# Optimization experiments

Measured on AMD Instinct MI355X. Metric: run time of the kernel, lower is better.

Reference implementation:

```python
import jax, jax.numpy as jnp
import numpy as np

NUM_HIST = 4
INTERVAL = 5
PROG_THRESH = 2.0

B = 32          # scenarios
AGENTS_PER = 10 # agents per scenario
A = B * AGENTS_PER
T = 32          # future intervals
P = 20000       # polylines
NG = 2000       # polygons
L = 180         # raw trajectory length (L//INTERVAL = 36 >= T+1)


def setup_inputs() -> dict:
    key = jax.random.key(0)
    ks = jax.random.split(key, 8)
    polyline_batch = jnp.sort(jax.random.randint(ks[0], (P,), 0, B, dtype=jnp.int32))
    polyline_position = jax.random.normal(ks[1], (P, 2), dtype=jnp.float32) * 50.0
    polyline_heading = jax.random.uniform(ks[2], (P,), dtype=jnp.float32) * 2.0 * np.pi
    edge_row1 = jax.random.randint(ks[3], (P,), 0, NG, dtype=jnp.int32)
    polyline_to_polygon_edge_index = jnp.stack([jnp.arange(P, dtype=jnp.int32), edge_row1])
    polygon_on_route_mask = jax.random.randint(ks[4], (NG,), 0, 2) > 0
    agent_ptr = (jnp.arange(B + 1, dtype=jnp.int32) * AGENTS_PER)
    agent_infer_position = jax.random.normal(ks[5], (A, NUM_HIST + T, 2), dtype=jnp.float32) * 50.0
    agent_batch = jnp.repeat(jnp.arange(B, dtype=jnp.int32), AGENTS_PER)
    agent_position = jax.random.normal(ks[6], (A, L, 2), dtype=jnp.float32) * 50.0
    return {
        "polyline_batch": polyline_batch,
        "polyline_position": polyline_position,
        "polyline_heading": polyline_heading,
        "polyline_to_polygon_edge_index": polyline_to_polygon_edge_index,
        "polygon_on_route_mask": polygon_on_route_mask,
        "agent_ptr": agent_ptr,
        "agent_infer_position": agent_infer_position,
        "agent_batch": agent_batch,
        "agent_position": agent_position,
    }


def _local_x(points, centers, cos_h, sin_h):
    # points [E,2]; centers [P,2]; returns x_local, y_local each [E,P]
    dx = points[:, None, 0] - centers[None, :, 0]
    dy = points[:, None, 1] - centers[None, :, 1]
    x = cos_h[None, :] * dx + sin_h[None, :] * dy
    y = -sin_h[None, :] * dx + cos_h[None, :] * dy
    return x, y


def _progress(pos, pos_pre, pos_batch, poly_pos, cos_h, sin_h, on_route, poly_batch, t):
    # dense equivalent of mask-build -> dense_to_sparse -> gather -> scatter_min
    x, y = _local_x(pos, poly_pos, cos_h, sin_h)          # [E,P]
    x_pre, _ = _local_x(pos_pre, poly_pos, cos_h, sin_h)  # [E,P]
    dist = jnp.abs(y) * 10.0 + jnp.abs(x) + jnp.where(x > 0, 1000.0, 0.0)
    valid = on_route[None, :] & (pos_batch[:, None] == poly_batch[None, :])
    dist = jnp.where(valid, dist, jnp.inf)
    j = jnp.argmin(dist, axis=1)                          # first-min, matches scatter_min
    has = jnp.any(valid, axis=1)
    x_sel = jnp.take_along_axis(x, j[:, None], axis=1)[:, 0]
    x_pre_sel = jnp.take_along_axis(x_pre, j[:, None], axis=1)[:, 0]
    prog = jnp.where(has, x_sel - x_pre_sel, 0.0)
    return prog.reshape(-1, t).sum(axis=-1)


def reference(polyline_batch, polyline_position, polyline_heading,
              polyline_to_polygon_edge_index, polygon_on_route_mask,
              agent_ptr, agent_infer_position, agent_batch, agent_position):
    poly_on_route = polygon_on_route_mask[polyline_to_polygon_edge_index[1]]
    cos_h = jnp.cos(polyline_heading)
    sin_h = jnp.sin(polyline_heading)

    ego_index = agent_ptr[:-1]
    ip = agent_infer_position[ego_index]                  # [B, NUM_HIST+T, 2]
    t = ip.shape[1] - NUM_HIST
    ego_pos = ip[:, NUM_HIST:].reshape(-1, 2)
    ego_pos_pre = ip[:, NUM_HIST - 1:-1].reshape(-1, 2)
    ego_b = jnp.repeat(agent_batch[ego_index], t)

    progress = _progress(ego_pos, ego_pos_pre, ego_b, polyline_position,
                         cos_h, sin_h, poly_on_route, polyline_batch, t)

    expert = agent_position[ego_index, ::INTERVAL]        # [B, L//INTERVAL, 2]
    expert_pre = expert[:, -t - 1:-1].reshape(-1, 2)
    expert_cur = expert[:, -t:].reshape(-1, 2)
    expert_progress = _progress(expert_cur, expert_pre, ego_b, polyline_position,
                                cos_h, sin_h, poly_on_route, polyline_batch, t)

    reward = jnp.minimum(
        jnp.maximum(progress, PROG_THRESH) / jnp.maximum(expert_progress, PROG_THRESH),
        1.0)
    return reward
```

## Files before the change

### kernel.cpp

```cpp
#include <hip/hip_runtime.h>

#define NUM_HIST 4
#define T_STEPS 32
#define B_BATCH 32
#define L_LEN 180
#define INTERVAL 5
#define CHUNK 2048
#define BT 1024

__global__ __launch_bounds__(BT) void fused_progress_reward(
    const int* __restrict__ pb,
    const float* __restrict__ pp,
    const float* __restrict__ hd,
    const int* __restrict__ edge,
    const unsigned int* __restrict__ mask,
    const int* __restrict__ aptr,
    const float* __restrict__ ipos,
    const int* __restrict__ abatch,
    const float* __restrict__ apos,
    float* __restrict__ out,
    int P)
{
    __shared__ float4 stage[CHUNK];
    __shared__ float progv[64];
    __shared__ int starts_sh[B_BATCH + 1];
    __shared__ int wcnt[16], woff[16];
    __shared__ int ccount_sh;

    const int tid = threadIdx.x;
    const int b   = blockIdx.x;

    bool bytemode = false;
    #pragma unroll
    for (int w = 0; w < 16; ++w) bytemode |= (mask[w] & 0xFFFFFF00u) != 0u;

    const int a  = aptr[b];
    const int bq = abatch[a];

    {
        int base = tid * 20;
        if (base < P) {
            int prev = (base == 0) ? -1 : pb[base - 1];
            int lim  = min(base + 20, P);
            for (int k = base; k + 3 < lim; k += 4) {
                int4 v4 = *(const int4*)(pb + k);
                int vals[4] = {v4.x, v4.y, v4.z, v4.w};
                #pragma unroll
                for (int u = 0; u < 4; ++u) {
                    int v = min(vals[u], B_BATCH);
                    for (int t = prev + 1; t <= v; ++t) starts_sh[t] = k + u;
                    prev = v;
                }
            }
            if (lim == P) {
                for (int t = prev + 1; t <= B_BATCH; ++t) starts_sh[t] = P;
            }
        }
        if (tid == 0) ccount_sh = 0;
    }

    const int qid = tid >> 4;
    const int sub = tid & 15;
    const int s   = qid >> 5;
    const int ts  = qid & 31;

    float cx, cy, px_, py_;
    if (s == 0) {
        const float2* base2 = (const float2*)(ipos + (size_t)a * ((NUM_HIST + T_STEPS) * 2));
        float2 pre = base2[NUM_HIST - 1 + ts];
        float2 cur = base2[NUM_HIST + ts];
        cx = cur.x; cy = cur.y; px_ = pre.x; py_ = pre.y;
    } else {
        const float2* base2 = (const float2*)(apos + (size_t)a * (L_LEN * 2));
        float2 pre = base2[(3 + ts) * INTERVAL];
        float2 cur = base2[(4 + ts) * INTERVAL];
        cx = cur.x; cy = cur.y; px_ = pre.x; py_ = pre.y;
    }

    __syncthreads();
    const int jb = starts_sh[bq];
    const int je = starts_sh[bq + 1];

    unsigned long long best = ~0ull;
    float bc = 0.0f, bs = 0.0f;
    int keybase = 0;

    const unsigned long long lt_mask = (1ull << (tid & 63)) - 1ull;

    for (int c0 = jb; c0 < je; c0 += CHUNK) {
        const int n = min(CHUNK, je - c0);

        for (int r0 = 0; r0 < n; r0 += BT) {
            int i = r0 + tid;
            bool on = false;
            float4 v;
            if (i < n) {
                int j = c0 + i;
                int g = edge[P + j];
                on = bytemode ? (((const unsigned char*)mask)[g] != 0)
                              : (mask[g] != 0u);
                float h  = hd[j];
                float cc = __cosf(h);
                float sn = __sinf(h);
                float2 p2 = ((const float2*)pp)[j];
                v = make_float4(cc, sn, cc * p2.x + sn * p2.y,
                                        -sn * p2.x + cc * p2.y);
            }
            unsigned long long bal = __ballot(on);
            int within = __popcll(bal & lt_mask);
            if ((tid & 63) == 0) wcnt[tid >> 6] = (int)__popcll(bal);
            __syncthreads();
            if (tid < 16) {
                int c = wcnt[tid];
                int p = c;
                #pragma unroll
                for (int off = 1; off < 16; off <<= 1) {
                    int t = __shfl_up(p, off, 64);
                    if (tid >= off) p += t;
                }
                int basev = ccount_sh;
                woff[tid] = basev + p - c;
                if (tid == 15) ccount_sh = basev + p;
            }
            __syncthreads();
            if (on) stage[woff[tid >> 6] + within] = v;
        }
        __syncthreads();
        const int nc = ccount_sh;

        for (int i = sub; i < nc; i += 16) {
            float4 e = stage[i];
            float x = e.x * cx + e.y * cy - e.z;
            float y = -e.y * cx + e.x * cy - e.w;
            float d = fabsf(y) * 10.0f + fabsf(x) + (x > 0.0f ? 1000.0f : 0.0f);
            unsigned long long cand =
                ((unsigned long long)__float_as_uint(d) << 32)
                | (unsigned int)(keybase + i);
            if (cand < best) { best = cand; bc = e.x; bs = e.y; }
        }
        keybase += nc;
        if (c0 + CHUNK < je) {
            __syncthreads();
            if (tid == 0) ccount_sh = 0;
        }
    }

    #pragma unroll
    for (int off = 1; off < 16; off <<= 1) {
        unsigned long long b2 = __shfl_xor(best, off, 64);
        float c2 = __shfl_xor(bc, off, 64);
        float s2 = __shfl_xor(bs, off, 64);
        if (b2 < best) { best = b2; bc = c2; bs = s2; }
    }

    if (sub == 0) {
        float prog = 0.0f;
        if (best != ~0ull)
            prog = bc * (cx - px_) + bs * (cy - py_);
        progv[qid] = prog;
    }
    __syncthreads();

    if (tid < 64) {
        float v = progv[tid];
        #pragma unroll
        for (int off = 16; off; off >>= 1) v += __shfl_xor(v, off, 64);
        float other = __shfl_xor(v, 32, 64);
        if (tid == 0)
            out[b] = fminf(fmaxf(v, 2.0f) / fmaxf(other, 2.0f), 1.0f);
    }
}

extern "C" void kernel_launch(void* const* d_in, const int* in_sizes, int n_in,
                              void* d_out, int out_size, void* d_ws, size_t ws_size,
                              hipStream_t stream) {
    const int*   poly_batch  = (const int*)d_in[0];
    const float* poly_pos    = (const float*)d_in[1];
    const float* heading     = (const float*)d_in[2];
    const int*   edge        = (const int*)d_in[3];
    const unsigned int* mask = (const unsigned int*)d_in[4];
    const int*   agent_ptr   = (const int*)d_in[5];
    const float* ipos        = (const float*)d_in[6];
    const int*   agent_batch = (const int*)d_in[7];
    const float* apos        = (const float*)d_in[8];
    float* out = (float*)d_out;

    const int P = in_sizes[0];

    fused_progress_reward<<<B_BATCH, BT, 0, stream>>>(
        poly_batch, poly_pos, heading, edge, mask,
        agent_ptr, ipos, agent_batch, apos, out, P);
}
```

Measured before the change: 75.38 us.

## Split into grid-wide prep kernel and lightweight per-scenario eval kernel

Moves the polyline transform, mask lookup and segment-start computation into a separate kernel that runs over all polylines with many blocks, writing transformed float4 records to workspace. Off-route polylines get a sentinel value that pushes their distance far above any real candidate, so the in-block ballot/prefix-sum compaction and its repeated barriers go away. The eval kernel then scans each scenario's range straight from global memory using 512 threads, 8 lanes per query. It recovers the heading from the winning index instead of carrying cos/sin through the reduction. The cost is a second launch and a workspace round trip, and the sentinel changes tie-breaking indices to global ones.

```diff
diff --git a/kernel.cpp b/kernel.cpp
--- a/kernel.cpp
+++ b/kernel.cpp
@@ -5,159 +5,116 @@
 #define B_BATCH 32
 #define L_LEN 180
 #define INTERVAL 5
-#define CHUNK 2048
-#define BT 1024
+#define PREP_BT 256
+#define EVAL_BT 512
 
-__global__ __launch_bounds__(BT) void fused_progress_reward(
+typedef unsigned long long u64;
+typedef unsigned int u32;
+
+__global__ __launch_bounds__(PREP_BT) void prep_kernel(
     const int* __restrict__ pb,
     const float* __restrict__ pp,
     const float* __restrict__ hd,
     const int* __restrict__ edge,
     const unsigned int* __restrict__ mask,
-    const int* __restrict__ aptr,
-    const float* __restrict__ ipos,
-    const int* __restrict__ abatch,
-    const float* __restrict__ apos,
-    float* __restrict__ out,
+    int* __restrict__ starts,
+    float4* __restrict__ tf,
     int P)
 {
-    __shared__ float4 stage[CHUNK];
-    __shared__ float progv[64];
-    __shared__ int starts_sh[B_BATCH + 1];
-    __shared__ int wcnt[16], woff[16];
-    __shared__ int ccount_sh;
-
-    const int tid = threadIdx.x;
-    const int b   = blockIdx.x;
-
     bool bytemode = false;
     #pragma unroll
     for (int w = 0; w < 16; ++w) bytemode |= (mask[w] & 0xFFFFFF00u) != 0u;
 
-    const int a  = aptr[b];
+    const int j = blockIdx.x * PREP_BT + threadIdx.x;
+    if (j >= P) return;
+
+    int g = edge[P + j];
+    bool on = bytemode ? (((const unsigned char*)mask)[g] != 0)
+                       : (mask[g] != 0u);
+    float4 v;
+    if (on) {
+        float h  = hd[j];
+        float cc = __cosf(h);
+        float sn = __sinf(h);
+        float2 p2 = ((const float2*)pp)[j];
+        v = make_float4(cc, sn, cc * p2.x + sn * p2.y,
+                                -sn * p2.x + cc * p2.y);
+    } else {
+        v = make_float4(0.0f, 0.0f, -3e30f, 0.0f);
+    }
+    tf[j] = v;
+
+    int val = min(pb[j], B_BATCH);
+    int pv  = (j == 0) ? -1 : min(pb[j - 1], B_BATCH);
+    for (int t = pv + 1; t <= val; ++t) starts[t] = j;
+    if (j == P - 1)
+        for (int t = val + 1; t <= B_BATCH; ++t) starts[t] = P;
+}
+
+__global__ __launch_bounds__(EVAL_BT) void eval_final_kernel(
+    const float4* __restrict__ tf,
+    const int* __restrict__ starts,
+    const int* __restrict__ aptr,
+    const int* __restrict__ abatch,
+    const float* __restrict__ ipos,
+    const float* __restrict__ apos,
+    const float* __restrict__ hd,
+    float* __restrict__ out)
+{
+    __shared__ float progv[64];
+
+    const int tid = threadIdx.x;
+    const int b   = blockIdx.x;
+    const int q   = tid >> 3;
+    const int sub = tid & 7;
+    const int s   = q >> 5;
+    const int ts  = q & 31;
+
+    const int a = aptr[b];
+    float2 pre, cur;
+    if (s == 0) {
+        const float2* b2 =
+            (const float2*)(ipos + (size_t)a * ((NUM_HIST + T_STEPS) * 2));
+        pre = b2[NUM_HIST - 1 + ts];
+        cur = b2[NUM_HIST + ts];
+    } else {
+        const float2* b2 = (const float2*)(apos + (size_t)a * (L_LEN * 2));
+        pre = b2[(3 + ts) * INTERVAL];
+        cur = b2[(4 + ts) * INTERVAL];
+    }
+    const float cx = cur.x, cy = cur.y;
+
     const int bq = abatch[a];
+    const int jb = starts[bq];
+    const int je = starts[bq + 1];
 
-    {
-        int base = tid * 20;
-        if (base < P) {
-            int prev = (base == 0) ? -1 : pb[base - 1];
-            int lim  = min(base + 20, P);
-            for (int k = base; k + 3 < lim; k += 4) {
-                int4 v4 = *(const int4*)(pb + k);
-                int vals[4] = {v4.x, v4.y, v4.z, v4.w};
-                #pragma unroll
-                for (int u = 0; u < 4; ++u) {
-                    int v = min(vals[u], B_BATCH);
-                    for (int t = prev + 1; t <= v; ++t) starts_sh[t] = k + u;
-                    prev = v;
-                }
-            }
-            if (lim == P) {
-                for (int t = prev + 1; t <= B_BATCH; ++t) starts_sh[t] = P;
-            }
-        }
-        if (tid == 0) ccount_sh = 0;
+    u64 best = ~0ull;
+    #pragma unroll 8
+    for (int i = jb + sub; i < je; i += 8) {
+        float4 e = tf[i];
+        float x =  e.x * cx + e.y * cy - e.z;
+        float y = -e.y * cx + e.x * cy - e.w;
+        float d = fabsf(y) * 10.0f + fabsf(x) + (x > 0.0f ? 1000.0f : 0.0f);
+        u64 cand = ((u64)__float_as_uint(d) << 32) | (u32)i;
+        if (cand < best) best = cand;
     }
 
-    const int qid = tid >> 4;
-    const int sub = tid & 15;
-    const int s   = qid >> 5;
-    const int ts  = qid & 31;
-
-    float cx, cy, px_, py_;
-    if (s == 0) {
-        const float2* base2 = (const float2*)(ipos + (size_t)a * ((NUM_HIST + T_STEPS) * 2));
-        float2 pre = base2[NUM_HIST - 1 + ts];
-        float2 cur = base2[NUM_HIST + ts];
-        cx = cur.x; cy = cur.y; px_ = pre.x; py_ = pre.y;
-    } else {
-        const float2* base2 = (const float2*)(apos + (size_t)a * (L_LEN * 2));
-        float2 pre = base2[(3 + ts) * INTERVAL];
-        float2 cur = base2[(4 + ts) * INTERVAL];
-        cx = cur.x; cy = cur.y; px_ = pre.x; py_ = pre.y;
-    }
-
-    __syncthreads();
-    const int jb = starts_sh[bq];
-    const int je = starts_sh[bq + 1];
-
-    unsigned long long best = ~0ull;
-    float bc = 0.0f, bs = 0.0f;
-    int keybase = 0;
-
-    const unsigned long long lt_mask = (1ull << (tid & 63)) - 1ull;
-
-    for (int c0 = jb; c0 < je; c0 += CHUNK) {
-        const int n = min(CHUNK, je - c0);
-
-        for (int r0 = 0; r0 < n; r0 += BT) {
-            int i = r0 + tid;
-            bool on = false;
-            float4 v;
-            if (i < n) {
-                int j = c0 + i;
-                int g = edge[P + j];
-                on = bytemode ? (((const unsigned char*)mask)[g] != 0)
-                              : (mask[g] != 0u);
-                float h  = hd[j];
-                float cc = __cosf(h);
-                float sn = __sinf(h);
-                float2 p2 = ((const float2*)pp)[j];
-                v = make_float4(cc, sn, cc * p2.x + sn * p2.y,
-                                        -sn * p2.x + cc * p2.y);
-            }
-            unsigned long long bal = __ballot(on);
-            int within = __popcll(bal & lt_mask);
-            if ((tid & 63) == 0) wcnt[tid >> 6] = (int)__popcll(bal);
-            __syncthreads();
-            if (tid < 16) {
-                int c = wcnt[tid];
-                int p = c;
-                #pragma unroll
-                for (int off = 1; off < 16; off <<= 1) {
-                    int t = __shfl_up(p, off, 64);
-                    if (tid >= off) p += t;
-                }
-                int basev = ccount_sh;
-                woff[tid] = basev + p - c;
-                if (tid == 15) ccount_sh = basev + p;
-            }
-            __syncthreads();
-            if (on) stage[woff[tid >> 6] + within] = v;
-        }
-        __syncthreads();
-        const int nc = ccount_sh;
-
-        for (int i = sub; i < nc; i += 16) {
-            float4 e = stage[i];
-            float x = e.x * cx + e.y * cy - e.z;
-            float y = -e.y * cx + e.x * cy - e.w;
-            float d = fabsf(y) * 10.0f + fabsf(x) + (x > 0.0f ? 1000.0f : 0.0f);
-            unsigned long long cand =
-                ((unsigned long long)__float_as_uint(d) << 32)
-                | (unsigned int)(keybase + i);
-            if (cand < best) { best = cand; bc = e.x; bs = e.y; }
-        }
-        keybase += nc;
-        if (c0 + CHUNK < je) {
-            __syncthreads();
-            if (tid == 0) ccount_sh = 0;
-        }
-    }
-
-    #pragma unroll
-    for (int off = 1; off < 16; off <<= 1) {
-        unsigned long long b2 = __shfl_xor(best, off, 64);
-        float c2 = __shfl_xor(bc, off, 64);
-        float s2 = __shfl_xor(bs, off, 64);
-        if (b2 < best) { best = b2; bc = c2; bs = s2; }
-    }
+    u64 o;
+    o = __shfl_xor(best, 1, 8); if (o < best) best = o;
+    o = __shfl_xor(best, 2, 8); if (o < best) best = o;
+    o = __shfl_xor(best, 4, 8); if (o < best) best = o;
 
     if (sub == 0) {
         float prog = 0.0f;
-        if (best != ~0ull)
-            prog = bc * (cx - px_) + bs * (cy - py_);
-        progv[qid] = prog;
+        if (best != ~0ull) {
+            float d = __uint_as_float((u32)(best >> 32));
+            if (d < 1e20f) {
+                int jw  = (int)(u32)best;
+                float h = hd[jw];
+                prog = __cosf(h) * (cx - pre.x) + __sinf(h) * (cy - pre.y);
+            }
+        }
+        progv[q] = prog;
     }
     __syncthreads();
 
@@ -186,8 +143,15 @@
     float* out = (float*)d_out;
 
     const int P = in_sizes[0];
+    const int scanB = (P + PREP_BT - 1) / PREP_BT;
 
-    fused_progress_reward<<<B_BATCH, BT, 0, stream>>>(
-        poly_batch, poly_pos, heading, edge, mask,
-        agent_ptr, ipos, agent_batch, apos, out, P);
+    char* ws = (char*)d_ws;
+    int*    starts = (int*)ws;
+    float4* tf     = (float4*)(ws + 256);
+
+    prep_kernel<<<scanB, PREP_BT, 0, stream>>>(
+        poly_batch, poly_pos, heading, edge, mask, starts, tf, P);
+
+    eval_final_kernel<<<B_BATCH, EVAL_BT, 0, stream>>>(
+        tf, starts, agent_ptr, agent_batch, ipos, apos, heading, out);
 }
```

Result: slower. 80.00 us (+6.1%).
